# Kernel tuning notes

Hardware: AMD Instinct MI355X
Metric: run time of the kernel (lower is better)

## Reference

```python
import jax, jax.numpy as jnp
import numpy as np
from jax import lax

B, FQ, T, H = 2, 257, 100, 96
S, DIN, N, R, KF, KM = 8, 192, 16, 6, 5, 4
GROUPS = 8

def _ln(x, g, b, eps=1e-5):
    m = x.mean(-1, keepdims=True)
    v = ((x - m) ** 2).mean(-1, keepdims=True)
    return (x - m) / jnp.sqrt(v + eps) * g + b

def _silu(x):
    return x * jax.nn.sigmoid(x)

def _fconv(x, g, b, cw, cb, alpha):
    Bb, Fq, Tt, Hh = x.shape
    y = _ln(x, g, b)  # LayerNorm over hidden dim H (seq_last=True path)
    y = y.transpose(0, 2, 3, 1).reshape(Bb * Tt, Hh, Fq)
    pad = (cw.shape[-1] - 1) // 2
    y = lax.conv_general_dilated(y, cw, (1,), [(pad, pad)],
                                 feature_group_count=GROUPS,
                                 dimension_numbers=('NCH', 'OIH', 'NCH')) + cb[:, None]
    y = jnp.where(y > 0, y, alpha[:, None] * y)  # PReLU per channel
    return y.reshape(Bb, Tt, Hh, Fq).transpose(0, 3, 1, 2)

def _full(x, g, b, sq_w, sq_b, fw, fb, uw, ub):
    Bb, Fq, Tt, Hh = x.shape
    y = _ln(x, g, b).transpose(0, 2, 3, 1).reshape(Bb * Tt, Hh, Fq)
    y = _silu(jnp.einsum('bhf,sh->bsf', y, sq_w) + sq_b[:, None])   # squeeze 1x1 conv
    y = jnp.einsum('bgf,gkf->bgk', y, fw) + fb                      # grouped full-band linear
    y = _silu(jnp.einsum('bsf,hs->bhf', y, uw) + ub[:, None])       # unsqueeze 1x1 conv
    return y.reshape(Bb, Tt, Hh, Fq).transpose(0, 3, 1, 2)

def _mamba(x, in_w, cw, cb, xp_w, dt_w, dt_b, A_log, Dp, out_w):
    # x: [Bm, T, H] -> Mamba selective scan (d_inner=DIN, d_state=N, dt_rank=R)
    Bm, Tt, Hh = x.shape
    xz = x @ in_w.T                                  # [Bm,T,2*DIN]
    xin, z = xz[..., :DIN], xz[..., DIN:]
    xc = xin.transpose(0, 2, 1)                      # [Bm,DIN,T]
    xc = lax.conv_general_dilated(xc, cw, (1,), [(KM - 1, 0)],
                                  feature_group_count=DIN,
                                  dimension_numbers=('NCH', 'OIH', 'NCH')) + cb[:, None]
    xc = _silu(xc).transpose(0, 2, 1)                # [Bm,T,DIN]
    dbl = xc @ xp_w.T                                # [Bm,T,R+2N]
    dt = jax.nn.softplus(dbl[..., :R] @ dt_w.T + dt_b)
    Bs, Cs = dbl[..., R:R + N], dbl[..., R + N:R + 2 * N]
    A = -jnp.exp(A_log)                              # [DIN,N]

    def step(h, inp):
        dt_t, x_t, B_t, C_t = inp
        h = jnp.exp(dt_t[..., None] * A) * h + (dt_t * x_t)[..., None] * B_t[:, None, :]
        return h, jnp.einsum('bdn,bn->bd', h, C_t)

    h0 = jnp.zeros((Bm, DIN, N), x.dtype)
    _, ys = lax.scan(step, h0, (dt.transpose(1, 0, 2), xc.transpose(1, 0, 2),
                                Bs.transpose(1, 0, 2), Cs.transpose(1, 0, 2)))
    y = ys.transpose(1, 0, 2) + xc * Dp
    return (y * _silu(z)) @ out_w.T

def setup_inputs():
    key = jax.random.key(0)
    ks = jax.random.split(key, 32)
    n = lambda i, shape, s=0.1: jax.random.normal(ks[i], shape) * s
    inp = dict(
        x=jax.random.normal(ks[0], (B, FQ, T, H)),
        ln1_g=jnp.ones((H,)), ln1_b=jnp.zeros((H,)),
        conv1_w=n(1, (H, H // GROUPS, KF), 0.2), conv1_b=n(2, (H,)),
        prelu1_a=jnp.full((H,), 0.25),
        lnf_g=jnp.ones((H,)), lnf_b=jnp.zeros((H,)),
        sq_w=n(3, (S, H)), sq_b=n(4, (S,)),
        full_w=n(5, (S, FQ, FQ), 0.06), full_b=n(6, (S, FQ)),
        unsq_w=n(7, (H, S), 0.3), unsq_b=n(8, (H,)),
        ln2_g=jnp.ones((H,)), ln2_b=jnp.zeros((H,)),
        conv2_w=n(9, (H, H // GROUPS, KF), 0.2), conv2_b=n(10, (H,)),
        prelu2_a=jnp.full((H,), 0.25),
        lnm_g=jnp.ones((H,)), lnm_b=jnp.zeros((H,)),
    )
    for p, off in (('m0_', 11), ('m1_', 21)):
        inp[p + 'in_w'] = n(off, (2 * DIN, H))
        inp[p + 'conv_w'] = n(off + 1, (DIN, 1, KM), 0.3)
        inp[p + 'conv_b'] = n(off + 2, (DIN,))
        inp[p + 'xp_w'] = n(off + 3, (R + 2 * N, DIN))
        inp[p + 'dt_w'] = n(off + 4, (DIN, R))
        inp[p + 'dt_b'] = n(off + 5, (DIN,)) - 2.0
        inp[p + 'A_log'] = jnp.log(jax.random.uniform(ks[off + 6], (DIN, N), minval=0.5, maxval=1.5))
        inp[p + 'D'] = jnp.ones((DIN,)) + n(off + 7, (DIN,))
        inp[p + 'out_w'] = n(off + 8, (H, DIN))
    return inp

def reference(x, ln1_g, ln1_b, conv1_w, conv1_b, prelu1_a,
              lnf_g, lnf_b, sq_w, sq_b, full_w, full_b, unsq_w, unsq_b,
              ln2_g, ln2_b, conv2_w, conv2_b, prelu2_a, lnm_g, lnm_b,
              m0_in_w, m0_conv_w, m0_conv_b, m0_xp_w, m0_dt_w, m0_dt_b, m0_A_log, m0_D, m0_out_w,
              m1_in_w, m1_conv_w, m1_conv_b, m1_xp_w, m1_dt_w, m1_dt_b, m1_A_log, m1_D, m1_out_w):
    x = x + _fconv(x, ln1_g, ln1_b, conv1_w, conv1_b, prelu1_a)
    x = x + _full(x, lnf_g, lnf_b, sq_w, sq_b, full_w, full_b, unsq_w, unsq_b)
    x = x + _fconv(x, ln2_g, ln2_b, conv2_w, conv2_b, prelu2_a)
    Bb, Fq, Tt, Hh = x.shape
    xn = _ln(x, lnm_g, lnm_b)
    yf = _mamba(xn.reshape(Bb * Fq, Tt, Hh),
                m0_in_w, m0_conv_w, m0_conv_b, m0_xp_w, m0_dt_w, m0_dt_b, m0_A_log, m0_D, m0_out_w)
    yb = _mamba(jnp.flip(xn, 2).reshape(Bb * Fq, Tt, Hh),
                m1_in_w, m1_conv_w, m1_conv_b, m1_xp_w, m1_dt_w, m1_dt_b, m1_A_log, m1_D, m1_out_w)
    x_fw = x + yf.reshape(Bb, Fq, Tt, Hh)
    x_bw = jnp.flip(x, 2) + yb.reshape(Bb, Fq, Tt, Hh)
    return (x_fw + jnp.flip(x_bw, 2)) / 2
```

## Files before the change

kernel.cpp:

```cpp
#include <hip/hip_runtime.h>
#include <math.h>

constexpr int kB   = 2;
constexpr int kF   = 257;
constexpr int kT   = 100;
constexpr int kH   = 96;
constexpr int kS   = 8;
constexpr int kD   = 192;
constexpr int kN   = 16;
constexpr int kR   = 6;
constexpr int kKF  = 5;
constexpr int kKM  = 4;
constexpr int kG   = 8;
constexpr int kGC  = kH / kG;
constexpr int kBM  = kB * kF;
constexpr int kROWS = kB * kF * kT;
constexpr int kNX  = kROWS * kH;
constexpr int kNM  = kROWS * kD;
constexpr int kDBL = kR + 2 * kN;
constexpr int kDBLP = 48;

__device__ inline float wave_reduce_sum(float v) {
    for (int o = 32; o > 0; o >>= 1) v += __shfl_xor(v, o, 64);
    return v;
}
__device__ inline float silu_f(float x) { return x / (1.f + __expf(-x)); }
__device__ inline float softplus_f(float x) { return x > 20.f ? x : log1pf(__expf(x)); }

__global__ void ln_kernel(const float* __restrict__ in, float* __restrict__ out,
                          const float* __restrict__ g, const float* __restrict__ b,
                          int rows) {
    int wave = threadIdx.x >> 6;
    int lane = threadIdx.x & 63;
    int r = blockIdx.x * 4 + wave;
    if (r >= rows) return;
    const float* p = in + (size_t)r * kH;
    float v0 = p[lane];
    float v1 = (lane < 32) ? p[64 + lane] : 0.f;
    float s = wave_reduce_sum(v0 + v1);
    float mean = s * (1.f / 96.f);
    float d0 = v0 - mean;
    float d1 = (lane < 32) ? (v1 - mean) : 0.f;
    float vs = wave_reduce_sum(d0 * d0 + d1 * d1);
    float rstd = rsqrtf(vs * (1.f / 96.f) + 1e-5f);
    float* q = out + (size_t)r * kH;
    q[lane] = d0 * rstd * g[lane] + b[lane];
    if (lane < 32) q[64 + lane] = d1 * rstd * g[64 + lane] + b[64 + lane];
}

#define FDOT(S,K) \
  acc += xw[S][0].x*wr[K][0] + xw[S][0].y*wr[K][1] + xw[S][0].z*wr[K][2] + xw[S][0].w*wr[K][3] \
       + xw[S][1].x*wr[K][4] + xw[S][1].y*wr[K][5] + xw[S][1].z*wr[K][6] + xw[S][1].w*wr[K][7] \
       + xw[S][2].x*wr[K][8] + xw[S][2].y*wr[K][9] + xw[S][2].z*wr[K][10]+ xw[S][2].w*wr[K][11];

#define FSTEP(S0,S1,S2,S3,S4)                                              \
  if (f < fmax) {                                                          \
    const float4* cp = (const float4*)(Xs + (f + 4) * 12);                 \
    xw[S4][0] = cp[0]; xw[S4][1] = cp[1]; xw[S4][2] = cp[2];               \
    float acc = bias;                                                      \
    FDOT(S0,0) FDOT(S1,1) FDOT(S2,2) FDOT(S3,3) FDOT(S4,4)                 \
    float yv = acc > 0.f ? acc : alpha_h * acc;                            \
    size_t oi = ((size_t)(bb * kF + f) * kT + tt) * kH + g12 + hh;         \
    out[oi] = resid[oi] + yv;                                              \
    f++;                                                                   \
  }

__global__ __launch_bounds__(256)
void fconv_kernel(const float* __restrict__ ln, const float* __restrict__ resid,
                  float* __restrict__ out, const float* __restrict__ w,
                  const float* __restrict__ cb, const float* __restrict__ alpha) {
    __shared__ float Xs[261 * 12];
    __shared__ float Ws[kGC * kKF * 12];
    int g = blockIdx.x, tt = blockIdx.y, bb = blockIdx.z;
    int g12 = g * 12;
    int tid = threadIdx.x;

    for (int i = tid; i < 720; i += 256) Ws[i] = w[g * 720 + i];
    for (int i = tid; i < 257 * 12; i += 256) {
        int fs = i / 12, ci = i - fs * 12;
        Xs[(fs + 2) * 12 + ci] = ln[((size_t)(bb * kF + fs) * kT + tt) * kH + g12 + ci];
    }
    if (tid < 48) {
        const int padr[4] = {0, 1, 259, 260};
        Xs[padr[tid / 12] * 12 + (tid % 12)] = 0.f;
    }
    __syncthreads();

    int lane = tid & 63, wave = tid >> 6;
    int hh = lane % 12, fi = lane / 12;
    if (fi >= 5) return;
    int slot = wave * 5 + fi;
    int f0 = slot * 13;
    int fmax = min(f0 + 13, kF);

    float wr[5][12];
    #pragma unroll
    for (int k = 0; k < 5; k++)
        #pragma unroll
        for (int ci = 0; ci < 12; ci++)
            wr[k][ci] = Ws[hh * 60 + ci * 5 + k];

    float bias = cb[g12 + hh];
    float alpha_h = alpha[g12 + hh];

    float4 xw[5][3];
    #pragma unroll
    for (int s = 0; s < 4; s++) {
        int row = min(f0 + s, 260);
        const float4* cp = (const float4*)(Xs + row * 12);
        xw[s][0] = cp[0]; xw[s][1] = cp[1]; xw[s][2] = cp[2];
    }
    int f = f0;
    for (int rep = 0; rep < 3; rep++) {
        FSTEP(0,1,2,3,4)
        FSTEP(1,2,3,4,0)
        FSTEP(2,3,4,0,1)
        FSTEP(3,4,0,1,2)
        FSTEP(4,0,1,2,3)
    }
}

__global__ void squeeze_kernel(const float* __restrict__ ln, float* __restrict__ s1,
                               const float* __restrict__ sqw, const float* __restrict__ sqb) {
    int bt = blockIdx.x;
    int f = blockIdx.y * 64 + threadIdx.x;
    if (f >= kF) return;
    int b = bt / kT, t = bt % kT;
    const float* row = ln + ((size_t)(b * kF + f) * kT + t) * kH;
    float acc[kS];
    for (int s = 0; s < kS; s++) acc[s] = 0.f;
    for (int h = 0; h < kH; h++) {
        float v = row[h];
        for (int s = 0; s < kS; s++) acc[s] += v * sqw[s * kH + h];
    }
    for (int s = 0; s < kS; s++)
        s1[((size_t)bt * kS + s) * kF + f] = silu_f(acc[s] + sqb[s]);
}

__global__ __launch_bounds__(256)
void fullmat_gemm(const float* __restrict__ s1, float* __restrict__ s2,
                  const float* __restrict__ fw, const float* __restrict__ fb) {
    __shared__ float As[64 * 64];
    __shared__ float Bs[64 * 64];
    int k0 = blockIdx.x * 64, bt0 = blockIdx.y * 64, g = blockIdx.z;
    int tid = threadIdx.x;
    int rt = tid >> 4, ct = tid & 15;
    float acc[4][4];
    #pragma unroll
    for (int i = 0; i < 4; i++)
        #pragma unroll
        for (int j = 0; j < 4; j++) acc[i][j] = 0.f;

    for (int f0 = 0; f0 < kF; f0 += 64) {
        int fcnt = min(64, kF - f0);
        for (int i = tid; i < 64 * 64; i += 256) {
            int m = i & 63, fk = i >> 6;
            int bt = bt0 + m, f = f0 + fk;
            As[fk * 64 + m] = (bt < kB * kT && f < kF)
                ? s1[((size_t)bt * kS + g) * kF + f] : 0.f;
            int k = k0 + m;
            Bs[fk * 64 + m] = (k < kF && f < kF)
                ? fw[(size_t)g * kF * kF + (size_t)k * kF + f] : 0.f;
        }
        __syncthreads();
        for (int f = 0; f < fcnt; f++) {
            float4 a4 = *(const float4*)&As[f * 64 + rt * 4];
            float4 b4 = *(const float4*)&Bs[f * 64 + ct * 4];
            float ar[4] = {a4.x, a4.y, a4.z, a4.w};
            float br[4] = {b4.x, b4.y, b4.z, b4.w};
            #pragma unroll
            for (int i = 0; i < 4; i++)
                #pragma unroll
                for (int j = 0; j < 4; j++) acc[i][j] += ar[i] * br[j];
        }
        __syncthreads();
    }
    #pragma unroll
    for (int i = 0; i < 4; i++) {
        int bt = bt0 + rt * 4 + i;
        if (bt >= kB * kT) continue;
        #pragma unroll
        for (int j = 0; j < 4; j++) {
            int k = k0 + ct * 4 + j;
            if (k >= kF) continue;
            s2[((size_t)bt * kS + g) * kF + k] = acc[i][j] + fb[g * kF + k];
        }
    }
}

__global__ void unsqueeze_kernel(const float* __restrict__ s2, float* __restrict__ x,
                                 const float* __restrict__ uw, const float* __restrict__ ub) {
    int idx = blockIdx.x * blockDim.x + threadIdx.x;
    if (idx >= kNX) return;
    int h = idx % kH;
    int t = (idx / kH) % kT;
    int f = (idx / (kH * kT)) % kF;
    int b = idx / (kH * kT * kF);
    int bt = b * kT + t;
    float acc = ub[h];
    for (int s = 0; s < kS; s++)
        acc += s2[((size_t)bt * kS + s) * kF + f] * uw[h * kS + s];
    x[idx] += silu_f(acc);
}

__global__ void transpose_kernel(const float* __restrict__ in, float* __restrict__ out,
                                 int rows, int cols) {
    int idx = blockIdx.x * blockDim.x + threadIdx.x;
    if (idx >= rows * cols) return;
    int r = idx / cols, c = idx % cols;
    out[c * rows + r] = in[idx];
}

__global__ void xppad_kernel(const float* __restrict__ w, float* __restrict__ wp) {
    int i = blockIdx.x * 256 + threadIdx.x;
    if (i >= kD * kDBLP) return;
    int d = i / kDBLP, n = i % kDBLP;
    wp[i] = (n < kDBL) ? w[n * kD + d] : 0.f;
}

__global__ __launch_bounds__(256)
void inproj_gemm(const float* __restrict__ xn, const float* __restrict__ wT,
                 float* __restrict__ xin, float* __restrict__ z) {
    __shared__ float Al[64 * 96];
    int r0 = blockIdx.x * 64;
    int c0 = blockIdx.y * 128;
    int tid = threadIdx.x;
    for (int i = tid; i < 64 * 24; i += 256) {
        int rr = i / 24, cq = i - rr * 24;
        int r = r0 + rr; if (r >= kROWS) r = kROWS - 1;
        *(float4*)&Al[rr * 96 + cq * 4] = *(const float4*)&xn[(size_t)r * kH + cq * 4];
    }
    __syncthreads();
    int rt = tid >> 5, ct = tid & 31;
    const float* ap = Al + rt * 8 * 96;
    const float* bp = wT + c0 + ct * 4;
    float4 acc[8];
    #pragma unroll
    for (int i = 0; i < 8; i++) acc[i] = make_float4(0.f, 0.f, 0.f, 0.f);
    for (int h = 0; h < 96; h++) {
        float4 b = *(const float4*)&bp[(size_t)h * 384];
        #pragma unroll
        for (int i = 0; i < 8; i++) {
            float av = ap[i * 96 + h];
            acc[i].x += av * b.x; acc[i].y += av * b.y;
            acc[i].z += av * b.z; acc[i].w += av * b.w;
        }
    }
    int cbase = c0 + ct * 4;
    #pragma unroll
    for (int i = 0; i < 8; i++) {
        int r = r0 + rt * 8 + i;
        if (r >= kROWS) break;
        if (cbase < kD) *(float4*)&xin[(size_t)r * kD + cbase] = acc[i];
        else            *(float4*)&z[(size_t)r * kD + cbase - kD] = acc[i];
    }
}

__global__ __launch_bounds__(256)
void outproj_gemm(const float* __restrict__ ym, const float* __restrict__ zg,
                  const float* __restrict__ wpT,
                  const float* __restrict__ xres, float* __restrict__ out, int dir) {
    __shared__ float Al[64 * 192];
    int r0 = blockIdx.x * 64;
    int tid = threadIdx.x;
    for (int i = tid; i < 64 * 48; i += 256) {
        int rr = i / 48, cq = i - rr * 48;
        int r = r0 + rr; if (r >= kROWS) r = kROWS - 1;
        size_t gidx = (size_t)r * kD + cq * 4;
        float4 a = *(const float4*)&ym[gidx];
        float4 g4 = *(const float4*)&zg[gidx];
        a.x *= silu_f(g4.x); a.y *= silu_f(g4.y);
        a.z *= silu_f(g4.z); a.w *= silu_f(g4.w);
        *(float4*)&Al[rr * 192 + cq * 4] = a;
    }
    __syncthreads();
    int rt = tid >> 5, ct = tid & 31;
    const float* ap = Al + rt * 8 * 192;
    const float* bp = wpT + ct * 3;
    float acc[8][3];
    #pragma unroll
    for (int i = 0; i < 8; i++) { acc[i][0] = 0.f; acc[i][1] = 0.f; acc[i][2] = 0.f; }
    for (int h = 0; h < 192; h++) {
        float b0 = bp[h * 96], b1 = bp[h * 96 + 1], b2 = bp[h * 96 + 2];
        #pragma unroll
        for (int i = 0; i < 8; i++) {
            float av = ap[i * 192 + h];
            acc[i][0] += av * b0; acc[i][1] += av * b1; acc[i][2] += av * b2;
        }
    }
    int cbase = ct * 3;
    #pragma unroll
    for (int i = 0; i < 8; i++) {
        int r = r0 + rt * 8 + i;
        if (r >= kROWS) break;
        size_t o = (size_t)r * kH + cbase;
        #pragma unroll
        for (int j = 0; j < 3; j++) {
            float base = dir ? out[o + j] : xres[o + j];
            out[o + j] = base + 0.5f * acc[i][j];
        }
    }
}

__global__ void mconv_kernel(const float* __restrict__ xin, float* __restrict__ xc,
                             const float* __restrict__ cw, const float* __restrict__ cb, int dir) {
    int qid = blockIdx.x * blockDim.x + threadIdx.x;
    if (qid >= kROWS * 48) return;
    int r = qid / 48, d4 = (qid - r * 48) * 4;
    int bm = r / kT, t = r - bm * kT;
    float4 acc = make_float4(cb[d4], cb[d4 + 1], cb[d4 + 2], cb[d4 + 3]);
    #pragma unroll
    for (int k = 0; k < kKM; k++) {
        int ts = dir ? (t + 3 - k) : (t + k - 3);
        if (ts < 0 || ts >= kT) continue;
        float4 v = *(const float4*)&xin[((size_t)bm * kT + ts) * kD + d4];
        acc.x += v.x * cw[(d4 + 0) * kKM + k];
        acc.y += v.y * cw[(d4 + 1) * kKM + k];
        acc.z += v.z * cw[(d4 + 2) * kKM + k];
        acc.w += v.w * cw[(d4 + 3) * kKM + k];
    }
    float4 o = make_float4(silu_f(acc.x), silu_f(acc.y), silu_f(acc.z), silu_f(acc.w));
    *(float4*)&xc[(size_t)r * kD + d4] = o;
}

__global__ __launch_bounds__(256)
void xpproj_gemm(const float* __restrict__ xc, float* __restrict__ dbl,
                 const float* __restrict__ wpx) {
    __shared__ float Al[64 * 192];
    int r0 = blockIdx.x * 64;
    int tid = threadIdx.x;
    for (int i = tid; i < 64 * 48; i += 256) {
        int rr = i / 48, cq = i - rr * 48;
        int r = r0 + rr; if (r >= kROWS) r = kROWS - 1;
        *(float4*)&Al[rr * 192 + cq * 4] = *(const float4*)&xc[(size_t)r * kD + cq * 4];
    }
    __syncthreads();
    int rt = tid >> 5, ct = tid & 31;
    if (ct >= 24) return;
    const float* ap = Al + rt * 8 * 192;
    const float* bp = wpx + ct * 2;
    float acc[8][2];
    #pragma unroll
    for (int i = 0; i < 8; i++) { acc[i][0] = 0.f; acc[i][1] = 0.f; }
    for (int h = 0; h < 192; h++) {
        float b0 = bp[h * kDBLP], b1 = bp[h * kDBLP + 1];
        #pragma unroll
        for (int i = 0; i < 8; i++) {
            float av = ap[i * 192 + h];
            acc[i][0] += av * b0; acc[i][1] += av * b1;
        }
    }
    int cbase = ct * 2;
    #pragma unroll
    for (int i = 0; i < 8; i++) {
        int r = r0 + rt * 8 + i;
        if (r >= kROWS) break;
        #pragma unroll
        for (int j = 0; j < 2; j++) {
            int c = cbase + j;
            if (c < kDBL) dbl[(size_t)r * kDBL + c] = acc[i][j];
        }
    }
}

__global__ __launch_bounds__(192)
void scan_kernel(const float* __restrict__ dbl, float* __restrict__ xcy,
                 const float* __restrict__ A_log, const float* __restrict__ dtw,
                 const float* __restrict__ dtb, const float* __restrict__ Dp, int dir) {
    int bm = blockIdx.x;
    int d = threadIdx.x;
    float A[kN], h[kN], dw[kR];
    #pragma unroll
    for (int n = 0; n < kN; n++) { A[n] = -__expf(A_log[d * kN + n]); h[n] = 0.f; }
    #pragma unroll
    for (int j = 0; j < kR; j++) dw[j] = dtw[d * kR + j];
    float db = dtb[d], Dv = Dp[d];

    const float* base = dbl + (size_t)bm * kT * kDBL;
    float* xrow = xcy + (size_t)bm * kT * kD + d;

    for (int tb = 0; tb < kT; tb += 4) {
        int ts[4];
        float xv[4];
        #pragma unroll
        for (int u = 0; u < 4; u++) {
            ts[u] = dir ? (kT - 1 - (tb + u)) : (tb + u);
            xv[u] = xrow[(size_t)ts[u] * kD];
        }
        #pragma unroll
        for (int u = 0; u < 4; u++) {
            const float* dr = base + ts[u] * kDBL;
            float s = db + dr[0] * dw[0] + dr[1] * dw[1] + dr[2] * dw[2]
                         + dr[3] * dw[3] + dr[4] * dw[4] + dr[5] * dw[5];
            float dt = softplus_f(s);
            float dtx = dt * xv[u];
            float y = 0.f;
            #pragma unroll
            for (int n = 0; n < kN; n++) {
                h[n] = __expf(dt * A[n]) * h[n] + dtx * dr[kR + n];
                y += h[n] * dr[kR + kN + n];
            }
            xrow[(size_t)ts[u] * kD] = y + xv[u] * Dv;
        }
    }
}

extern "C" void kernel_launch(void* const* d_in, const int* in_sizes, int n_in,
                              void* d_out, int out_size, void* d_ws, size_t ws_size,
                              hipStream_t stream) {
    const float* x       = (const float*)d_in[0];
    const float* ln1_g   = (const float*)d_in[1];
    const float* ln1_b   = (const float*)d_in[2];
    const float* conv1_w = (const float*)d_in[3];
    const float* conv1_b = (const float*)d_in[4];
    const float* prelu1  = (const float*)d_in[5];
    const float* lnf_g   = (const float*)d_in[6];
    const float* lnf_b   = (const float*)d_in[7];
    const float* sq_w    = (const float*)d_in[8];
    const float* sq_b    = (const float*)d_in[9];
    const float* full_w  = (const float*)d_in[10];
    const float* full_b  = (const float*)d_in[11];
    const float* unsq_w  = (const float*)d_in[12];
    const float* unsq_b  = (const float*)d_in[13];
    const float* ln2_g   = (const float*)d_in[14];
    const float* ln2_b   = (const float*)d_in[15];
    const float* conv2_w = (const float*)d_in[16];
    const float* conv2_b = (const float*)d_in[17];
    const float* prelu2  = (const float*)d_in[18];
    const float* lnm_g   = (const float*)d_in[19];
    const float* lnm_b   = (const float*)d_in[20];

    float* ws   = (float*)d_ws;
    float* xbuf = ws;
    float* xn   = ws + (size_t)kNX;
    float* bufA = ws + 2 * (size_t)kNX;
    float* bufB = bufA + (size_t)kNM;
    float* bufC = bufB + (size_t)kNM;
    float* wTs  = bufC + (size_t)kNM;
    float* in_wT[2]  = { wTs, wTs + 2 * kD * kH };
    float* out_wp[2] = { wTs + 2 * (2 * kD * kH),
                         wTs + 2 * (2 * kD * kH) + kD * kH };
    float* xp_wp[2]  = { wTs + 2 * (2 * kD * kH) + 2 * kD * kH,
                         wTs + 2 * (2 * kD * kH) + 2 * kD * kH + kD * kDBLP };

    for (int dir = 0; dir < 2; dir++) {
        int wi = 21 + dir * 9;
        const float* in_w  = (const float*)d_in[wi + 0];
        const float* xp_w  = (const float*)d_in[wi + 3];
        const float* out_w = (const float*)d_in[wi + 8];
        transpose_kernel<<<(2 * kD * kH + 255) / 256, 256, 0, stream>>>(in_w, in_wT[dir], 2 * kD, kH);
        transpose_kernel<<<(kH * kD + 255) / 256, 256, 0, stream>>>(out_w, out_wp[dir], kH, kD);
        xppad_kernel<<<(kD * kDBLP + 255) / 256, 256, 0, stream>>>(xp_w, xp_wp[dir]);
    }

    int lnGrid = (kROWS + 3) / 4;
    int nxGrid = (kNX + 255) / 256;
    dim3 fcGrid(kG, kT, kB);

    ln_kernel<<<lnGrid, 256, 0, stream>>>(x, bufA, ln1_g, ln1_b, kROWS);
    fconv_kernel<<<fcGrid, 256, 0, stream>>>(bufA, x, xbuf, conv1_w, conv1_b, prelu1);

    ln_kernel<<<lnGrid, 256, 0, stream>>>(xbuf, bufA, lnf_g, lnf_b, kROWS);
    squeeze_kernel<<<dim3(kB * kT, (kF + 63) / 64), 64, 0, stream>>>(bufA, bufB, sq_w, sq_b);
    fullmat_gemm<<<dim3(5, 4, kS), 256, 0, stream>>>(bufB, bufC, full_w, full_b);
    unsqueeze_kernel<<<nxGrid, 256, 0, stream>>>(bufC, xbuf, unsq_w, unsq_b);

    ln_kernel<<<lnGrid, 256, 0, stream>>>(xbuf, bufA, ln2_g, ln2_b, kROWS);
    fconv_kernel<<<fcGrid, 256, 0, stream>>>(bufA, xbuf, xbuf, conv2_w, conv2_b, prelu2);

    ln_kernel<<<lnGrid, 256, 0, stream>>>(xbuf, xn, lnm_g, lnm_b, kROWS);

    for (int dir = 0; dir < 2; dir++) {
        int wi = 21 + dir * 9;
        const float* conv_w = (const float*)d_in[wi + 1];
        const float* conv_b = (const float*)d_in[wi + 2];
        const float* dt_w   = (const float*)d_in[wi + 4];
        const float* dt_b   = (const float*)d_in[wi + 5];
        const float* A_log  = (const float*)d_in[wi + 6];
        const float* Dp     = (const float*)d_in[wi + 7];

        inproj_gemm<<<dim3((kROWS + 63) / 64, 3), 256, 0, stream>>>(xn, in_wT[dir], bufA, bufB);
        mconv_kernel<<<(kROWS * 48 + 255) / 256, 256, 0, stream>>>(bufA, bufC, conv_w, conv_b, dir);
        xpproj_gemm<<<(kROWS + 63) / 64, 256, 0, stream>>>(bufC, bufA, xp_wp[dir]);
        scan_kernel<<<kBM, kD, 0, stream>>>(bufA, bufC, A_log, dt_w, dt_b, Dp, dir);
        outproj_gemm<<<(kROWS + 63) / 64, 256, 0, stream>>>(bufC, bufB, out_wp[dir], xbuf, (float*)d_out, dir);
    }
}
```

Measured before the change: 946.1 us.

## Run both Mamba direction scans in one batched launch

The forward and backward Mamba pipelines now keep their intermediates in separate buffers, and a new scan2_kernel processes both directions in a single 2-D grid. This doubles the number of scan blocks per launch so the sequential-in-time scan can fill more of the GPU instead of running as two half-sized launches back to back. It needs two extra workspace buffers and reuses the xn region for the dbl outputs. When the workspace is too small it falls back to the original per-direction loop.

```diff
diff --git a/kernel.cpp b/kernel.cpp
--- a/kernel.cpp
+++ b/kernel.cpp
@@ -364,9 +364,22 @@
 }
 
 __global__ __launch_bounds__(192)
-void scan_kernel(const float* __restrict__ dbl, float* __restrict__ xcy,
-                 const float* __restrict__ A_log, const float* __restrict__ dtw,
-                 const float* __restrict__ dtb, const float* __restrict__ Dp, int dir) {
+void scan2_kernel(const float* __restrict__ dbl0, const float* __restrict__ dbl1,
+                  float* __restrict__ xc0, float* __restrict__ xc1,
+                  const float* __restrict__ Al0, const float* __restrict__ Al1,
+                  const float* __restrict__ dtw0, const float* __restrict__ dtw1,
+                  const float* __restrict__ dtb0, const float* __restrict__ dtb1,
+                  const float* __restrict__ Dp0, const float* __restrict__ Dp1,
+                  int dirbase) {
+    int dd = blockIdx.y;
+    int dir = dirbase + dd;
+    const float* dbl   = dd ? dbl1 : dbl0;
+    float* xcy         = dd ? xc1  : xc0;
+    const float* A_log = dd ? Al1  : Al0;
+    const float* dtw   = dd ? dtw1 : dtw0;
+    const float* dtb   = dd ? dtb1 : dtb0;
+    const float* Dp    = dd ? Dp1  : Dp0;
+
     int bm = blockIdx.x;
     int d = threadIdx.x;
     float A[kN], h[kN], dw[kR];
@@ -433,56 +446,82 @@
     float* ws   = (float*)d_ws;
     float* xbuf = ws;
     float* xn   = ws + (size_t)kNX;
-    float* bufA = ws + 2 * (size_t)kNX;
-    float* bufB = bufA + (size_t)kNM;
-    float* bufC = bufB + (size_t)kNM;
-    float* wTs  = bufC + (size_t)kNM;
+    float* R1   = xn + (size_t)kNX;
+    float* R2   = R1 + (size_t)kNM;
+    float* R3   = R2 + (size_t)kNM;
+    float* wTs  = R3 + (size_t)kNM;
     float* in_wT[2]  = { wTs, wTs + 2 * kD * kH };
     float* out_wp[2] = { wTs + 2 * (2 * kD * kH),
                          wTs + 2 * (2 * kD * kH) + kD * kH };
     float* xp_wp[2]  = { wTs + 2 * (2 * kD * kH) + 2 * kD * kH,
                          wTs + 2 * (2 * kD * kH) + 2 * kD * kH + kD * kDBLP };
-
+    float* wEnd = wTs + 2 * (2 * kD * kH) + 2 * kD * kH + 2 * kD * kDBLP;
+    float* R4 = wEnd;
+    float* R5 = R4 + (size_t)kNM;
+    size_t need_batched = (size_t)((R5 + (size_t)kNM) - ws) * sizeof(float);
+    bool batched = (ws_size >= need_batched);
+
+    const float* mw[2][8];
     for (int dir = 0; dir < 2; dir++) {
         int wi = 21 + dir * 9;
-        const float* in_w  = (const float*)d_in[wi + 0];
-        const float* xp_w  = (const float*)d_in[wi + 3];
-        const float* out_w = (const float*)d_in[wi + 8];
-        transpose_kernel<<<(2 * kD * kH + 255) / 256, 256, 0, stream>>>(in_w, in_wT[dir], 2 * kD, kH);
-        transpose_kernel<<<(kH * kD + 255) / 256, 256, 0, stream>>>(out_w, out_wp[dir], kH, kD);
-        xppad_kernel<<<(kD * kDBLP + 255) / 256, 256, 0, stream>>>(xp_w, xp_wp[dir]);
+        mw[dir][0] = (const float*)d_in[wi + 1];
+        mw[dir][1] = (const float*)d_in[wi + 2];
+        mw[dir][2] = (const float*)d_in[wi + 4];
+        mw[dir][3] = (const float*)d_in[wi + 5];
+        mw[dir][4] = (const float*)d_in[wi + 6];
+        mw[dir][5] = (const float*)d_in[wi + 7];
+        transpose_kernel<<<(2 * kD * kH + 255) / 256, 256, 0, stream>>>(
+            (const float*)d_in[wi + 0], in_wT[dir], 2 * kD, kH);
+        transpose_kernel<<<(kH * kD + 255) / 256, 256, 0, stream>>>(
+            (const float*)d_in[wi + 8], out_wp[dir], kH, kD);
+        xppad_kernel<<<(kD * kDBLP + 255) / 256, 256, 0, stream>>>(
+            (const float*)d_in[wi + 3], xp_wp[dir]);
     }
 
     int lnGrid = (kROWS + 3) / 4;
     int nxGrid = (kNX + 255) / 256;
     dim3 fcGrid(kG, kT, kB);
-
-    ln_kernel<<<lnGrid, 256, 0, stream>>>(x, bufA, ln1_g, ln1_b, kROWS);
-    fconv_kernel<<<fcGrid, 256, 0, stream>>>(bufA, x, xbuf, conv1_w, conv1_b, prelu1);
-
-    ln_kernel<<<lnGrid, 256, 0, stream>>>(xbuf, bufA, lnf_g, lnf_b, kROWS);
-    squeeze_kernel<<<dim3(kB * kT, (kF + 63) / 64), 64, 0, stream>>>(bufA, bufB, sq_w, sq_b);
-    fullmat_gemm<<<dim3(5, 4, kS), 256, 0, stream>>>(bufB, bufC, full_w, full_b);
-    unsqueeze_kernel<<<nxGrid, 256, 0, stream>>>(bufC, xbuf, unsq_w, unsq_b);
-
-    ln_kernel<<<lnGrid, 256, 0, stream>>>(xbuf, bufA, ln2_g, ln2_b, kROWS);
-    fconv_kernel<<<fcGrid, 256, 0, stream>>>(bufA, xbuf, xbuf, conv2_w, conv2_b, prelu2);
+    int gemmGrid = (kROWS + 63) / 64;
+    int mcGrid = (kROWS * 48 + 255) / 256;
+
+    ln_kernel<<<lnGrid, 256, 0, stream>>>(x, R1, ln1_g, ln1_b, kROWS);
+    fconv_kernel<<<fcGrid, 256, 0, stream>>>(R1, x, xbuf, conv1_w, conv1_b, prelu1);
+
+    ln_kernel<<<lnGrid, 256, 0, stream>>>(xbuf, R1, lnf_g, lnf_b, kROWS);
+    squeeze_kernel<<<dim3(kB * kT, (kF + 63) / 64), 64, 0, stream>>>(R1, R2, sq_w, sq_b);
+    fullmat_gemm<<<dim3(5, 4, kS), 256, 0, stream>>>(R2, R3, full_w, full_b);
+    unsqueeze_kernel<<<nxGrid, 256, 0, stream>>>(R3, xbuf, unsq_w, unsq_b);
+
+    ln_kernel<<<lnGrid, 256, 0, stream>>>(xbuf, R1, ln2_g, ln2_b, kROWS);
+    fconv_kernel<<<fcGrid, 256, 0, stream>>>(R1, xbuf, xbuf, conv2_w, conv2_b, prelu2);
 
     ln_kernel<<<lnGrid, 256, 0, stream>>>(xbuf, xn, lnm_g, lnm_b, kROWS);
 
-    for (int dir = 0; dir < 2; dir++) {
-        int wi = 21 + dir * 9;
-        const float* conv_w = (const float*)d_in[wi + 1];
-        const float* conv_b = (const float*)d_in[wi + 2];
-        const float* dt_w   = (const float*)d_in[wi + 4];
-        const float* dt_b   = (const float*)d_in[wi + 5];
-        const float* A_log  = (const float*)d_in[wi + 6];
-        const float* Dp     = (const float*)d_in[wi + 7];
-
-        inproj_gemm<<<dim3((kROWS + 63) / 64, 3), 256, 0, stream>>>(xn, in_wT[dir], bufA, bufB);
-        mconv_kernel<<<(kROWS * 48 + 255) / 256, 256, 0, stream>>>(bufA, bufC, conv_w, conv_b, dir);
-        xpproj_gemm<<<(kROWS + 63) / 64, 256, 0, stream>>>(bufC, bufA, xp_wp[dir]);
-        scan_kernel<<<kBM, kD, 0, stream>>>(bufA, bufC, A_log, dt_w, dt_b, Dp, dir);
-        outproj_gemm<<<(kROWS + 63) / 64, 256, 0, stream>>>(bufC, bufB, out_wp[dir], xbuf, (float*)d_out, dir);
-    }
-}
+    if (batched) {
+        float* dbl0 = xn;
+        float* dbl1 = xn + (size_t)kROWS * kDBL;
+        inproj_gemm<<<dim3(gemmGrid, 3), 256, 0, stream>>>(xn, in_wT[0], R1, R2);
+        mconv_kernel<<<mcGrid, 256, 0, stream>>>(R1, R4, mw[0][0], mw[0][1], 0);
+        inproj_gemm<<<dim3(gemmGrid, 3), 256, 0, stream>>>(xn, in_wT[1], R1, R3);
+        mconv_kernel<<<mcGrid, 256, 0, stream>>>(R1, R5, mw[1][0], mw[1][1], 1);
+        xpproj_gemm<<<gemmGrid, 256, 0, stream>>>(R4, dbl0, xp_wp[0]);
+        xpproj_gemm<<<gemmGrid, 256, 0, stream>>>(R5, dbl1, xp_wp[1]);
+        scan2_kernel<<<dim3(kBM, 2), 192, 0, stream>>>(
+            dbl0, dbl1, R4, R5,
+            mw[0][4], mw[1][4], mw[0][2], mw[1][2],
+            mw[0][3], mw[1][3], mw[0][5], mw[1][5], 0);
+        outproj_gemm<<<gemmGrid, 256, 0, stream>>>(R4, R2, out_wp[0], xbuf, (float*)d_out, 0);
+        outproj_gemm<<<gemmGrid, 256, 0, stream>>>(R5, R3, out_wp[1], xbuf, (float*)d_out, 1);
+    } else {
+        for (int dir = 0; dir < 2; dir++) {
+            inproj_gemm<<<dim3(gemmGrid, 3), 256, 0, stream>>>(xn, in_wT[dir], R1, R2);
+            mconv_kernel<<<mcGrid, 256, 0, stream>>>(R1, R3, mw[dir][0], mw[dir][1], dir);
+            xpproj_gemm<<<gemmGrid, 256, 0, stream>>>(R3, R1, xp_wp[dir]);
+            scan2_kernel<<<dim3(kBM, 1), 192, 0, stream>>>(
+                R1, R1, R3, R3,
+                mw[dir][4], mw[dir][4], mw[dir][2], mw[dir][2],
+                mw[dir][3], mw[dir][3], mw[dir][5], mw[dir][5], dir);
+            outproj_gemm<<<gemmGrid, 256, 0, stream>>>(R3, R2, out_wp[dir], xbuf, (float*)d_out, dir);
+        }
+    }
+}
```

Measured after the change: 887.1 us. 1.07x faster.
